# Performance work log

Measured on AMD Instinct MI355X. Metric: run time of the kernel, lower is better.

Reference implementation:

```python
import jax, jax.numpy as jnp
import numpy as np

N_HEAD = 16
N_KV_HEAD = 4


def setup_inputs() -> dict:
    key = jax.random.key(0)
    ks = jax.random.split(key, 5)
    B, T, D = 2, 2048, 2048
    kdim = D // N_HEAD  # 128
    s = 0.02
    x = jax.random.normal(ks[0], (B, T, D), dtype=jnp.float32)
    Wq = jax.random.normal(ks[1], (D, D), dtype=jnp.float32) * s
    Wk = jax.random.normal(ks[2], (D, N_KV_HEAD * kdim), dtype=jnp.float32) * s
    Wv = jax.random.normal(ks[3], (D, N_KV_HEAD * kdim), dtype=jnp.float32) * s
    Wo = jax.random.normal(ks[4], (D, D), dtype=jnp.float32) * s
    return {"x": x, "Wq": Wq, "Wk": Wk, "Wv": Wv, "Wo": Wo}


def reference(x, Wq, Wk, Wv, Wo):
    B, T, D = x.shape
    h, kv = N_HEAD, N_KV_HEAD
    g = h // kv  # query groups per kv head
    kdim = D // h
    Q = (x @ Wq).reshape(B, T, h, kdim).transpose(0, 2, 1, 3)   # [B,h,T,k]
    K = (x @ Wk).reshape(B, T, kv, kdim).transpose(0, 2, 1, 3)  # [B,kv,T,k]
    V = (x @ Wv).reshape(B, T, kv, kdim).transpose(0, 2, 1, 3)
    # repeat_interleave(g, dim=1): kv outer, group inner
    K = jnp.broadcast_to(K[:, :, None], (B, kv, g, T, kdim)).reshape(B, h, T, kdim)
    V = jnp.broadcast_to(V[:, :, None], (B, kv, g, T, kdim)).reshape(B, h, T, kdim)
    scores = jnp.einsum('bhqd,bhkd->bhqk', Q, K) / jnp.sqrt(jnp.float32(kdim))
    causal = jnp.tril(jnp.ones((T, T), dtype=bool))
    scores = jnp.where(causal[None, None], scores, jnp.float32(-jnp.inf))
    A = jax.nn.softmax(scores, axis=-1)
    Y = jnp.einsum('bhqk,bhkd->bhqd', A, V).transpose(0, 2, 1, 3).reshape(B, T, D)
    return Y @ Wo
```

## Files before the change

### kernel.cpp

```cpp
#include <hip/hip_runtime.h>
#include <hip/hip_bf16.h>

typedef __bf16 bf16x8 __attribute__((ext_vector_type(8)));
typedef float f32x4 __attribute__((ext_vector_type(4)));

__device__ __forceinline__ unsigned short f2bf(float f) {
  unsigned int u = __float_as_uint(f);
  u += 0x7fffu + ((u >> 16) & 1u);
  return (unsigned short)(u >> 16);
}

__device__ __forceinline__ unsigned int pack2(float lo, float hi) {
  __hip_bfloat162 h = __float22bfloat162_rn(float2{lo, hi});
  return *(unsigned int*)&h;
}

__device__ __forceinline__ void load_lds16(const void* g, void* l) {
  __builtin_amdgcn_global_load_lds(
      (const __attribute__((address_space(1))) unsigned int*)g,
      (__attribute__((address_space(3))) unsigned int*)l, 16, 0, 0);
}

__global__ void cvt_x(const float* __restrict__ in, unsigned short* __restrict__ out) {
  size_t i = ((size_t)blockIdx.x * 256 + threadIdx.x) * 4;
  float4 v = *(const float4*)(in + i);
  ushort4 o;
  o.x = f2bf(v.x); o.y = f2bf(v.y); o.z = f2bf(v.z); o.w = f2bf(v.w);
  *(ushort4*)(out + i) = o;
}

__global__ void tr_w(const float* __restrict__ in, unsigned short* __restrict__ out,
                     int ldin, int ldout) {
  __shared__ float tile[32][33];
  const int c0 = blockIdx.x * 32, r0 = blockIdx.y * 32;
  const int tx = threadIdx.x, ty = threadIdx.y;
#pragma unroll
  for (int j = 0; j < 4; ++j)
    tile[ty + j * 8][tx] = in[(size_t)(r0 + ty + j * 8) * ldin + c0 + tx];
  __syncthreads();
#pragma unroll
  for (int j = 0; j < 4; ++j)
    out[(size_t)(c0 + ty + j * 8) * ldout + r0 + tx] = f2bf(tile[tx][ty + j * 8]);
}

__global__ void tr_v(const unsigned short* __restrict__ QKV, unsigned short* __restrict__ VT) {
  __shared__ unsigned short tile[32][33];
  const int z = blockIdx.z, b = z >> 2, kvh = z & 3;
  const unsigned short* in = QKV + (size_t)(b * 2048) * 3072 + 2560 + kvh * 128;
  unsigned short* out = VT + (size_t)z * 128 * 2048;
  const int c0 = blockIdx.x * 32, r0 = blockIdx.y * 32;
  const int tx = threadIdx.x, ty = threadIdx.y;
#pragma unroll
  for (int j = 0; j < 4; ++j)
    tile[ty + j * 8][tx] = in[(size_t)(r0 + ty + j * 8) * 3072 + c0 + tx];
  __syncthreads();
#pragma unroll
  for (int j = 0; j < 4; ++j)
    out[(size_t)(c0 + ty + j * 8) * 2048 + r0 + tx] = tile[tx][ty + j * 8];
}

template <int OUTF32>
__global__ void gemm_bt(const unsigned short* __restrict__ A,
                        const unsigned short* __restrict__ B,
                        void* __restrict__ Cv, int M, int N, int K) {
  __shared__ __attribute__((aligned(16))) unsigned short As[128 * 64];
  __shared__ __attribute__((aligned(16))) unsigned short Bs[128 * 64];
  const int tid = threadIdx.x;
  const int lane = tid & 63;
  const int cl = lane & 15, rg = lane >> 4;
  const int wave = tid >> 6;
  const int bm = blockIdx.y, bn = blockIdx.x;
  const int wm = wave >> 1, wn = wave & 1;
  f32x4 acc[4][4] = {};
  const int nk = K >> 6;
  for (int kt = 0; kt < nk; ++kt) {
    const int k0 = kt << 6;
    __syncthreads();
#pragma unroll
    for (int i = 0; i < 8; ++i) {
      const int Ls = (i & 3) * 256 + tid;
      const int r = Ls >> 3, s = Ls & 7;
      const int c = s ^ (r & 7);
      const unsigned short* src;
      unsigned short* dst;
      if (i < 4) {
        src = A + (size_t)(bm * 128 + r) * K + k0 + c * 8;
        dst = As + (((i & 3) * 256 + (tid & 0xC0)) << 3);
      } else {
        src = B + (size_t)(bn * 128 + r) * K + k0 + c * 8;
        dst = Bs + (((i & 3) * 256 + (tid & 0xC0)) << 3);
      }
      load_lds16(src, dst);
    }
    __syncthreads();
#pragma unroll
    for (int ks = 0; ks < 2; ++ks) {
      bf16x8 af[4], bfr[4];
#pragma unroll
      for (int m = 0; m < 4; ++m) {
        const int row = wm * 64 + m * 16 + cl;
        const int p = (ks * 4 + rg) ^ (row & 7);
        af[m] = *(const bf16x8*)(As + row * 64 + p * 8);
      }
#pragma unroll
      for (int n = 0; n < 4; ++n) {
        const int row = wn * 64 + n * 16 + cl;
        const int p = (ks * 4 + rg) ^ (row & 7);
        bfr[n] = *(const bf16x8*)(Bs + row * 64 + p * 8);
      }
#pragma unroll
      for (int m = 0; m < 4; ++m)
#pragma unroll
        for (int n = 0; n < 4; ++n)
          acc[m][n] = __builtin_amdgcn_mfma_f32_16x16x32_bf16(af[m], bfr[n], acc[m][n], 0, 0, 0);
    }
  }
#pragma unroll
  for (int m = 0; m < 4; ++m)
#pragma unroll
    for (int n = 0; n < 4; ++n)
#pragma unroll
      for (int i = 0; i < 4; ++i) {
        const int row = bm * 128 + wm * 64 + m * 16 + rg * 4 + i;
        const int col = bn * 128 + wn * 64 + n * 16 + cl;
        if (OUTF32)
          ((float*)Cv)[(size_t)row * N + col] = acc[m][n][i];
        else
          ((unsigned short*)Cv)[(size_t)row * N + col] = f2bf(acc[m][n][i]);
      }
}

__global__ __launch_bounds__(256, 2) void attn(const unsigned short* __restrict__ QKV,
                                               const unsigned short* __restrict__ VT,
                                               unsigned short* __restrict__ O) {
  __shared__ __attribute__((aligned(16))) unsigned short Ks[2][64 * 128];
  __shared__ __attribute__((aligned(16))) unsigned short VTs[2][128 * 64];
  const int T = 2048, LD = 3072, D = 2048;
  const int jp = blockIdx.x, h = blockIdx.y, b = blockIdx.z;
  const int kvh = h >> 2;
  const int tid = threadIdx.x, lane = tid & 63, wave = tid >> 6;
  const int cl = lane & 15, rg = lane >> 4;
  const bool abit = (lane & 16) != 0, bbit = (lane & 32) != 0;
  const bool ab = abit != bbit;
  const unsigned short* Kbase = QKV + (size_t)b * T * LD + 2048 + kvh * 128;
  const unsigned short* Vbase = VT + (size_t)(b * 4 + kvh) * 128 * T;

  auto stage = [&](int sb, int k0) {
#pragma unroll
    for (int i = 0; i < 4; ++i) {
      const int Ls = i * 256 + tid;
      const int r = Ls >> 4, s = Ls & 15, c = s ^ (r & 7);
      load_lds16(Kbase + (size_t)(k0 + r) * LD + c * 8,
                 &Ks[sb][(i * 256 + (tid & 0xC0)) * 8]);
    }
#pragma unroll
    for (int i = 0; i < 4; ++i) {
      const int Ls = i * 256 + tid;
      const int r = Ls >> 3, s = Ls & 7, c = s ^ (r & 7);
      load_lds16(Vbase + (size_t)r * T + k0 + c * 8,
                 &VTs[sb][(i * 256 + (tid & 0xC0)) * 8]);
    }
  };

  const float scale = 0.08838834764831845f;

#pragma unroll 1
  for (int pass = 0; pass < 2; ++pass) {
    const int jt = pass ? (31 - jp) : jp;
    const int q0 = jt * 64;
    const int nkt = jt + 1;
    const int qrow = q0 + wave * 16 + cl;

    const unsigned short* Qp = QKV + (size_t)(b * T + qrow) * LD + h * 128;
    bf16x8 qf[4];
#pragma unroll
    for (int ks = 0; ks < 4; ++ks) qf[ks] = *(const bf16x8*)(Qp + ks * 32 + rg * 8);

    f32x4 o[8] = {};
    float m = -1e30f, l = 0.f;
    int buf = 0;

    stage(0, 0);
    __syncthreads();

#pragma unroll 1
    for (int kt = 0; kt < nkt; ++kt) {
      if (kt + 1 < nkt) stage(buf ^ 1, (kt + 1) * 64);

      f32x4 sa[4] = {};
      __builtin_amdgcn_s_setprio(1);
#pragma unroll
      for (int ks = 0; ks < 4; ++ks) {
#pragma unroll
        for (int n = 0; n < 4; ++n) {
          const int row = n * 16 + cl;
          const int p = (ks * 4 + rg) ^ (row & 7);
          const bf16x8 kf = *(const bf16x8*)(&Ks[buf][row * 128 + p * 8]);
          sa[n] = __builtin_amdgcn_mfma_f32_16x16x32_bf16(kf, qf[ks], sa[n], 0, 0, 0);
        }
      }
      __builtin_amdgcn_s_setprio(0);

      const int k0 = kt * 64;
      float p[4][4];
      float pmax = -1e30f;
      if (kt == jt) {
#pragma unroll
        for (int n = 0; n < 4; ++n)
#pragma unroll
          for (int i = 0; i < 4; ++i) {
            const int kg = k0 + n * 16 + rg * 4 + i;
            p[n][i] = (kg > qrow) ? -1e30f : sa[n][i] * scale;
            pmax = fmaxf(pmax, p[n][i]);
          }
      } else {
#pragma unroll
        for (int n = 0; n < 4; ++n)
#pragma unroll
          for (int i = 0; i < 4; ++i) {
            p[n][i] = sa[n][i] * scale;
            pmax = fmaxf(pmax, p[n][i]);
          }
      }
      pmax = fmaxf(pmax, __shfl_xor(pmax, 16));
      pmax = fmaxf(pmax, __shfl_xor(pmax, 32));

      if (!__all(pmax <= m + 8.f)) {
        const float mnew = fmaxf(m, pmax);
        const float alpha = __expf(m - mnew);
        m = mnew;
        l *= alpha;
#pragma unroll
        for (int n2 = 0; n2 < 8; ++n2) o[n2] *= alpha;
      }

      float rs = 0.f;
#pragma unroll
      for (int n = 0; n < 4; ++n)
#pragma unroll
        for (int i = 0; i < 4; ++i) {
          p[n][i] = __expf(p[n][i] - m);
          rs += p[n][i];
        }
      rs += __shfl_xor(rs, 16);
      rs += __shfl_xor(rs, 32);
      l += rs;

      unsigned int F[2][4];
#pragma unroll
      for (int ks2 = 0; ks2 < 2; ++ks2) {
        const unsigned int pk00 = pack2(p[2 * ks2][0], p[2 * ks2][1]);
        const unsigned int pk01 = pack2(p[2 * ks2][2], p[2 * ks2][3]);
        const unsigned int pk10 = pack2(p[2 * ks2 + 1][0], p[2 * ks2 + 1][1]);
        const unsigned int pk11 = pack2(p[2 * ks2 + 1][2], p[2 * ks2 + 1][3]);
        const unsigned int s0 = bbit ? pk00 : pk10;
        const unsigned int s1 = bbit ? pk01 : pk11;
        const unsigned int r0 = (unsigned int)__shfl_xor((int)s0, 32);
        const unsigned int r1 = (unsigned int)__shfl_xor((int)s1, 32);
        const unsigned int gk0 = bbit ? pk10 : pk00;
        const unsigned int gk1 = bbit ? pk11 : pk01;
        const unsigned int t0 = ab ? gk0 : r0;
        const unsigned int t1 = ab ? gk1 : r1;
        const unsigned int u0 = (unsigned int)__shfl_xor((int)t0, 16);
        const unsigned int u1 = (unsigned int)__shfl_xor((int)t1, 16);
        const unsigned int k20 = ab ? r0 : gk0;
        const unsigned int k21 = ab ? r1 : gk1;
        F[ks2][0] = abit ? u0 : k20;
        F[ks2][1] = abit ? u1 : k21;
        F[ks2][2] = abit ? k20 : u0;
        F[ks2][3] = abit ? k21 : u1;
      }

      __builtin_amdgcn_s_setprio(1);
#pragma unroll
      for (int ks2 = 0; ks2 < 2; ++ks2) {
        uint4 fu = make_uint4(F[ks2][0], F[ks2][1], F[ks2][2], F[ks2][3]);
        const bf16x8 pf = *(const bf16x8*)&fu;
#pragma unroll
        for (int n2 = 0; n2 < 8; ++n2) {
          const int dr = n2 * 16 + cl;
          const int p2 = (ks2 * 4 + rg) ^ (dr & 7);
          const bf16x8 vf = *(const bf16x8*)(&VTs[buf][dr * 64 + p2 * 8]);
          o[n2] = __builtin_amdgcn_mfma_f32_16x16x32_bf16(vf, pf, o[n2], 0, 0, 0);
        }
      }
      __builtin_amdgcn_s_setprio(0);

      __syncthreads();
      buf ^= 1;
    }

    const float rl = __builtin_amdgcn_rcpf(l);
#pragma unroll
    for (int n2 = 0; n2 < 8; ++n2) {
      ushort4 ov;
      ov.x = f2bf(o[n2][0] * rl);
      ov.y = f2bf(o[n2][1] * rl);
      ov.z = f2bf(o[n2][2] * rl);
      ov.w = f2bf(o[n2][3] * rl);
      *(ushort4*)(O + (size_t)(b * T + qrow) * D + h * 128 + n2 * 16 + rg * 4) = ov;
    }
  }
}

extern "C" void kernel_launch(void* const* d_in, const int* in_sizes, int n_in,
                              void* d_out, int out_size, void* d_ws, size_t ws_size,
                              hipStream_t stream) {
  const float* x = (const float*)d_in[0];
  const float* Wq = (const float*)d_in[1];
  const float* Wk = (const float*)d_in[2];
  const float* Wv = (const float*)d_in[3];
  const float* Wo = (const float*)d_in[4];
  float* out = (float*)d_out;

  char* ws = (char*)d_ws;
  unsigned short* xb    = (unsigned short*)(ws);
  unsigned short* WqkvT = (unsigned short*)(ws + 16777216);
  unsigned short* WoT   = (unsigned short*)(ws + 29360128);
  unsigned short* QKV   = (unsigned short*)(ws + 37748736);
  unsigned short* VTb   = (unsigned short*)(ws + 62914560);

  cvt_x<<<dim3(8192), dim3(256), 0, stream>>>(x, xb);
  tr_w<<<dim3(64, 64), dim3(32, 8), 0, stream>>>(Wq, WqkvT, 2048, 2048);
  tr_w<<<dim3(16, 64), dim3(32, 8), 0, stream>>>(Wk, WqkvT + (size_t)2048 * 2048, 512, 2048);
  tr_w<<<dim3(16, 64), dim3(32, 8), 0, stream>>>(Wv, WqkvT + (size_t)2560 * 2048, 512, 2048);
  tr_w<<<dim3(64, 64), dim3(32, 8), 0, stream>>>(Wo, WoT, 2048, 2048);

  gemm_bt<0><<<dim3(24, 32), dim3(256), 0, stream>>>(xb, WqkvT, QKV, 4096, 3072, 2048);
  tr_v<<<dim3(4, 64, 8), dim3(32, 8), 0, stream>>>(QKV, VTb);
  attn<<<dim3(16, 16, 2), dim3(256), 0, stream>>>(QKV, VTb, xb);
  gemm_bt<1><<<dim3(16, 32), dim3(256), 0, stream>>>(xb, WoT, out, 4096, 2048, 2048);
}
```

Measured before the change: 201.1 us.

## Replace GEMMs with 256-row tiled pipelined kernel and use exp2 softmax with MFMA row sums

Both projection GEMMs switch to a new 512-thread kernel with a 256-row tile, double-buffered LDS split into two K halves, explicit vmcnt waits and barriers, so global loads overlap the MFMA work and each block reuses more data. The attention kernel folds log2(e) into the scale so it can use exp2f, and it computes the softmax row sum with an extra MFMA against a ones vector instead of shuffle reductions. The lazy rescale threshold is raised to stay consistent with the base-2 scale. The risks are higher register pressure from the larger accumulator tiles and a slightly different accumulation order for the row sum, which is computed from bf16-rounded probabilities.

```diff
diff --git a/kernel.cpp b/kernel.cpp
--- a/kernel.cpp
+++ b/kernel.cpp
@@ -59,74 +59,122 @@
     out[(size_t)(c0 + ty + j * 8) * 2048 + r0 + tx] = tile[tx][ty + j * 8];
 }
 
-template <int OUTF32>
-__global__ void gemm_bt(const unsigned short* __restrict__ A,
-                        const unsigned short* __restrict__ B,
-                        void* __restrict__ Cv, int M, int N, int K) {
-  __shared__ __attribute__((aligned(16))) unsigned short As[128 * 64];
-  __shared__ __attribute__((aligned(16))) unsigned short Bs[128 * 64];
+template <int NF, int OUTF32>
+__global__ __launch_bounds__(512, 2) void gemm256(const unsigned short* __restrict__ A,
+                                                  const unsigned short* __restrict__ B,
+                                                  void* __restrict__ Cv, int M, int N, int K) {
+  __shared__ __attribute__((aligned(16))) unsigned short Ah[2][2][256 * 32];
+  __shared__ __attribute__((aligned(16))) unsigned short Bf[2][64 * NF * 64];
   const int tid = threadIdx.x;
   const int lane = tid & 63;
   const int cl = lane & 15, rg = lane >> 4;
   const int wave = tid >> 6;
+  const int wm = wave >> 2, wn = wave & 3;
   const int bm = blockIdx.y, bn = blockIdx.x;
-  const int wm = wave >> 1, wn = wave & 1;
-  f32x4 acc[4][4] = {};
-  const int nk = K >> 6;
-  for (int kt = 0; kt < nk; ++kt) {
-    const int k0 = kt << 6;
-    __syncthreads();
-#pragma unroll
-    for (int i = 0; i < 8; ++i) {
-      const int Ls = (i & 3) * 256 + tid;
-      const int r = Ls >> 3, s = Ls & 7;
-      const int c = s ^ (r & 7);
-      const unsigned short* src;
-      unsigned short* dst;
-      if (i < 4) {
-        src = A + (size_t)(bm * 128 + r) * K + k0 + c * 8;
-        dst = As + (((i & 3) * 256 + (tid & 0xC0)) << 3);
-      } else {
-        src = B + (size_t)(bn * 128 + r) * K + k0 + c * 8;
-        dst = Bs + (((i & 3) * 256 + (tid & 0xC0)) << 3);
-      }
-      load_lds16(src, dst);
-    }
-    __syncthreads();
-#pragma unroll
-    for (int ks = 0; ks < 2; ++ks) {
-      bf16x8 af[4], bfr[4];
-#pragma unroll
-      for (int m = 0; m < 4; ++m) {
-        const int row = wm * 64 + m * 16 + cl;
-        const int p = (ks * 4 + rg) ^ (row & 7);
-        af[m] = *(const bf16x8*)(As + row * 64 + p * 8);
-      }
-#pragma unroll
-      for (int n = 0; n < 4; ++n) {
-        const int row = wn * 64 + n * 16 + cl;
-        const int p = (ks * 4 + rg) ^ (row & 7);
-        bfr[n] = *(const bf16x8*)(Bs + row * 64 + p * 8);
-      }
-#pragma unroll
-      for (int m = 0; m < 4; ++m)
-#pragma unroll
-        for (int n = 0; n < 4; ++n)
-          acc[m][n] = __builtin_amdgcn_mfma_f32_16x16x32_bf16(af[m], bfr[n], acc[m][n], 0, 0, 0);
-    }
+  const int NK = K >> 6;
+  const int rowA = bm * 256, rowB = bn * (64 * NF);
+
+  f32x4 acc[8][NF] = {};
+
+  auto stage_A = [&](int bf, int h, int kt) {
+#pragma unroll
+    for (int i = 0; i < 2; ++i) {
+      const int L = i * 512 + tid;
+      const int r = L >> 2;
+      const int c = (L & 3) ^ ((r >> 1) & 3);
+      load_lds16(A + (size_t)(rowA + r) * K + kt * 64 + h * 32 + c * 8,
+                 &Ah[bf][h][(size_t)(i * 512 + (tid & ~63)) * 8]);
+    }
+  };
+  auto stage_B = [&](int bf, int kt) {
+#pragma unroll
+    for (int i = 0; i < NF; ++i) {
+      const int L = i * 512 + tid;
+      const int r = L >> 3;
+      const int c = (L & 7) ^ (r & 7);
+      load_lds16(B + (size_t)(rowB + r) * K + kt * 64 + c * 8,
+                 &Bf[bf][(size_t)(i * 512 + (tid & ~63)) * 8]);
+    }
+  };
+
+  stage_B(0, 0);
+  stage_A(0, 0, 0);
+  stage_A(0, 1, 0);
+  asm volatile("s_waitcnt vmcnt(2)" ::: "memory");
+  __builtin_amdgcn_s_barrier();
+
+  int buf = 0;
+#pragma unroll 1
+  for (int kt = 0; kt < NK; ++kt) {
+    const bool nl = (kt + 1 < NK);
+    bf16x8 af[8], bfr[NF];
+
+#pragma unroll
+    for (int f = 0; f < 8; ++f) {
+      const int r = 128 * wm + 16 * f + cl;
+      af[f] = *(const bf16x8*)(&Ah[buf][0][(r * 4 + (rg ^ ((r >> 1) & 3))) * 8]);
+    }
+#pragma unroll
+    for (int nf = 0; nf < NF; ++nf) {
+      const int r = 16 * NF * wn + 16 * nf + cl;
+      bfr[nf] = *(const bf16x8*)(&Bf[buf][(r * 8 + (rg ^ (r & 7))) * 8]);
+    }
+    if (nl) stage_B(buf ^ 1, kt + 1);
+    __builtin_amdgcn_s_barrier();
+    asm volatile("s_waitcnt lgkmcnt(0)" ::: "memory");
+    __builtin_amdgcn_s_setprio(1);
+#pragma unroll
+    for (int f = 0; f < 8; ++f)
+#pragma unroll
+      for (int nf = 0; nf < NF; ++nf)
+        acc[f][nf] = __builtin_amdgcn_mfma_f32_16x16x32_bf16(af[f], bfr[nf], acc[f][nf], 0, 0, 0);
+    __builtin_amdgcn_s_setprio(0);
+    if (nl) {
+      if constexpr (NF == 3) { asm volatile("s_waitcnt vmcnt(3)" ::: "memory"); }
+      else                   { asm volatile("s_waitcnt vmcnt(2)" ::: "memory"); }
+    } else {
+      asm volatile("s_waitcnt vmcnt(0)" ::: "memory");
+    }
+    __builtin_amdgcn_s_barrier();
+
+#pragma unroll
+    for (int f = 0; f < 8; ++f) {
+      const int r = 128 * wm + 16 * f + cl;
+      af[f] = *(const bf16x8*)(&Ah[buf][1][(r * 4 + (rg ^ ((r >> 1) & 3))) * 8]);
+    }
+#pragma unroll
+    for (int nf = 0; nf < NF; ++nf) {
+      const int r = 16 * NF * wn + 16 * nf + cl;
+      bfr[nf] = *(const bf16x8*)(&Bf[buf][(r * 8 + ((4 + rg) ^ (r & 7))) * 8]);
+    }
+    if (nl) { stage_A(buf ^ 1, 0, kt + 1); stage_A(buf ^ 1, 1, kt + 1); }
+    __builtin_amdgcn_s_barrier();
+    asm volatile("s_waitcnt lgkmcnt(0)" ::: "memory");
+    __builtin_amdgcn_s_setprio(1);
+#pragma unroll
+    for (int f = 0; f < 8; ++f)
+#pragma unroll
+      for (int nf = 0; nf < NF; ++nf)
+        acc[f][nf] = __builtin_amdgcn_mfma_f32_16x16x32_bf16(af[f], bfr[nf], acc[f][nf], 0, 0, 0);
+    __builtin_amdgcn_s_setprio(0);
+    if (nl) asm volatile("s_waitcnt vmcnt(2)" ::: "memory");
+    __builtin_amdgcn_s_barrier();
+
+    buf ^= 1;
   }
-#pragma unroll
-  for (int m = 0; m < 4; ++m)
-#pragma unroll
-    for (int n = 0; n < 4; ++n)
+
+#pragma unroll
+  for (int f = 0; f < 8; ++f)
+#pragma unroll
+    for (int nf = 0; nf < NF; ++nf)
 #pragma unroll
       for (int i = 0; i < 4; ++i) {
-        const int row = bm * 128 + wm * 64 + m * 16 + rg * 4 + i;
-        const int col = bn * 128 + wn * 64 + n * 16 + cl;
+        const int row = bm * 256 + wm * 128 + f * 16 + rg * 4 + i;
+        const int col = bn * 64 * NF + wn * 16 * NF + nf * 16 + cl;
         if (OUTF32)
-          ((float*)Cv)[(size_t)row * N + col] = acc[m][n][i];
+          ((float*)Cv)[(size_t)row * N + col] = acc[f][nf][i];
         else
-          ((unsigned short*)Cv)[(size_t)row * N + col] = f2bf(acc[m][n][i]);
+          ((unsigned short*)Cv)[(size_t)row * N + col] = f2bf(acc[f][nf][i]);
       }
 }
 
@@ -162,7 +210,9 @@
     }
   };
 
-  const float scale = 0.08838834764831845f;
+  const float scale2 = 0.12751742929f;
+  const uint4 onesu = make_uint4(0x3F803F80u, 0x3F803F80u, 0x3F803F80u, 0x3F803F80u);
+  const bf16x8 ones = *(const bf16x8*)&onesu;
 
 #pragma unroll 1
   for (int pass = 0; pass < 2; ++pass) {
@@ -177,7 +227,8 @@
     for (int ks = 0; ks < 4; ++ks) qf[ks] = *(const bf16x8*)(Qp + ks * 32 + rg * 8);
 
     f32x4 o[8] = {};
-    float m = -1e30f, l = 0.f;
+    f32x4 ol = {};
+    float m = -1e30f;
     int buf = 0;
 
     stage(0, 0);
@@ -210,7 +261,7 @@
 #pragma unroll
           for (int i = 0; i < 4; ++i) {
             const int kg = k0 + n * 16 + rg * 4 + i;
-            p[n][i] = (kg > qrow) ? -1e30f : sa[n][i] * scale;
+            p[n][i] = (kg > qrow) ? -1e30f : sa[n][i] * scale2;
             pmax = fmaxf(pmax, p[n][i]);
           }
       } else {
@@ -218,33 +269,27 @@
         for (int n = 0; n < 4; ++n)
 #pragma unroll
           for (int i = 0; i < 4; ++i) {
-            p[n][i] = sa[n][i] * scale;
+            p[n][i] = sa[n][i] * scale2;
             pmax = fmaxf(pmax, p[n][i]);
           }
       }
       pmax = fmaxf(pmax, __shfl_xor(pmax, 16));
       pmax = fmaxf(pmax, __shfl_xor(pmax, 32));
 
-      if (!__all(pmax <= m + 8.f)) {
+      if (!__all(pmax <= m + 11.0f)) {
         const float mnew = fmaxf(m, pmax);
-        const float alpha = __expf(m - mnew);
+        const float alpha = exp2f(m - mnew);
         m = mnew;
-        l *= alpha;
+        ol *= alpha;
 #pragma unroll
         for (int n2 = 0; n2 < 8; ++n2) o[n2] *= alpha;
       }
 
-      float rs = 0.f;
 #pragma unroll
       for (int n = 0; n < 4; ++n)
 #pragma unroll
-        for (int i = 0; i < 4; ++i) {
-          p[n][i] = __expf(p[n][i] - m);
-          rs += p[n][i];
-        }
-      rs += __shfl_xor(rs, 16);
-      rs += __shfl_xor(rs, 32);
-      l += rs;
+        for (int i = 0; i < 4; ++i)
+          p[n][i] = exp2f(p[n][i] - m);
 
       unsigned int F[2][4];
 #pragma unroll
@@ -276,6 +321,7 @@
       for (int ks2 = 0; ks2 < 2; ++ks2) {
         uint4 fu = make_uint4(F[ks2][0], F[ks2][1], F[ks2][2], F[ks2][3]);
         const bf16x8 pf = *(const bf16x8*)&fu;
+        ol = __builtin_amdgcn_mfma_f32_16x16x32_bf16(ones, pf, ol, 0, 0, 0);
 #pragma unroll
         for (int n2 = 0; n2 < 8; ++n2) {
           const int dr = n2 * 16 + cl;
@@ -290,7 +336,7 @@
       buf ^= 1;
     }
 
-    const float rl = __builtin_amdgcn_rcpf(l);
+    const float rl = __builtin_amdgcn_rcpf(ol[0]);
 #pragma unroll
     for (int n2 = 0; n2 < 8; ++n2) {
       ushort4 ov;
@@ -326,8 +372,8 @@
   tr_w<<<dim3(16, 64), dim3(32, 8), 0, stream>>>(Wv, WqkvT + (size_t)2560 * 2048, 512, 2048);
   tr_w<<<dim3(64, 64), dim3(32, 8), 0, stream>>>(Wo, WoT, 2048, 2048);
 
-  gemm_bt<0><<<dim3(24, 32), dim3(256), 0, stream>>>(xb, WqkvT, QKV, 4096, 3072, 2048);
+  gemm256<3, 0><<<dim3(16, 16), dim3(512), 0, stream>>>(xb, WqkvT, QKV, 4096, 3072, 2048);
   tr_v<<<dim3(4, 64, 8), dim3(32, 8), 0, stream>>>(QKV, VTb);
   attn<<<dim3(16, 16, 2), dim3(256), 0, stream>>>(QKV, VTb, xb);
-  gemm_bt<1><<<dim3(16, 32), dim3(256), 0, stream>>>(xb, WoT, out, 4096, 2048, 2048);
-}
+  gemm256<2, 1><<<dim3(16, 16), dim3(512), 0, stream>>>(xb, WoT, out, 4096, 2048, 2048);
+}
```

New measurement: 195.9 us. -2.6%, faster.
